# Kernel optimization log

Measured on AMD Instinct MI355X. Metric: run time of the kernel, lower is better.

## Reference

```python
import jax, jax.numpy as jnp
import numpy as np

N = 10000
E = 320000
NFEAT = 512
NHID = 256
NCLASS = 64
N_LAYERS = 8
ALPHA = 0.1
THETA = 0.5
BN_EPS = 1e-5


def setup_inputs() -> dict:
    key = jax.random.key(0)
    k = jax.random.split(key, 6)
    return {
        "x": jax.random.normal(k[0], (N, NFEAT), jnp.float32),
        "edge_index": jax.random.randint(k[1], (2, E), 0, N, dtype=jnp.int32),
        "lin0_w": jax.random.normal(k[2], (NFEAT, NHID), jnp.float32) * float(1.0 / np.sqrt(NFEAT)),
        "lin0_b": jnp.zeros((NHID,), jnp.float32),
        "lin1_w": jax.random.normal(k[3], (NHID, NCLASS), jnp.float32) * float(1.0 / np.sqrt(NHID)),
        "lin1_b": jnp.zeros((NCLASS,), jnp.float32),
        "conv_w": jax.random.normal(k[4], (N_LAYERS, NHID, NHID), jnp.float32) * float(1.0 / np.sqrt(NHID)),
        "bn_gamma": jnp.ones((N_LAYERS, NHID), jnp.float32),
        "bn_beta": jnp.zeros((N_LAYERS, NHID), jnp.float32),
    }


def reference(x, edge_index, lin0_w, lin0_b, lin1_w, lin1_b, conv_w, bn_gamma, bn_beta):
    # gcn_norm with self-loops: D^{-1/2} (A + I) D^{-1/2}
    loops = jnp.arange(N, dtype=edge_index.dtype)
    row = jnp.concatenate([edge_index[0], loops])
    col = jnp.concatenate([edge_index[1], loops])
    deg = jax.ops.segment_sum(jnp.ones_like(row, dtype=x.dtype), col, num_segments=N)
    dinv = jnp.where(deg > 0, jax.lax.rsqrt(jnp.maximum(deg, 1e-12)), 0.0)
    ew = dinv[row] * dinv[col]  # [E+N] edge weights

    def spmm(h):
        # adj_t built with (row=col, col=row): out[col[e]] += w[e] * h[row[e]]
        return jax.ops.segment_sum(ew[:, None] * h[row], col, num_segments=N)

    h = jax.nn.relu(x @ lin0_w + lin0_b)  # [N, NHID]
    x0 = h

    layer_idx = jnp.arange(1, N_LAYERS + 1, dtype=x.dtype)
    betas = jnp.log(THETA / layer_idx + 1.0)  # GCN2Conv beta per layer

    def step(h, layer):
        Wl, g, b, beta = layer
        p = spmm(h)
        p = (1.0 - ALPHA) * p + ALPHA * x0  # initial residual blend
        out = (1.0 - beta) * p + beta * (p @ Wl)  # identity mapping
        mu = out.mean(axis=0)
        var = out.var(axis=0)
        out = (out - mu) * jax.lax.rsqrt(var + BN_EPS) * g + b
        return jax.nn.relu(out), None

    h, _ = jax.lax.scan(step, h, (conv_w, bn_gamma, bn_beta, betas))
    return h @ lin1_w + lin1_b  # [N, NCLASS]
```

## Files before the change

kernel.cpp:

```cpp
#include <hip/hip_runtime.h>
#include <hip/hip_fp16.h>
#include <math.h>

#define N_NODES 10000
#define N_EDGES 320000
#define NFEAT 512
#define NHID 256
#define NCLASS 64
#define N_LAYERS 8
#define BN_EPS 1e-5f

typedef unsigned short u16;
typedef __attribute__((ext_vector_type(8))) short short8v;
typedef __attribute__((ext_vector_type(4))) float f32x4;

__device__ __forceinline__ u16 bf_hi_bits(float f) {
    unsigned u = __float_as_uint(f);
    unsigned r = (u + 0x7fffu + ((u >> 16) & 1u)) >> 16;
    return (u16)r;
}
__device__ __forceinline__ float bf_to_f(u16 h) {
    return __uint_as_float(((unsigned)h) << 16);
}
__device__ __forceinline__ float4 loadh4(const __half* p) {
    float2 raw = *(const float2*)p;
    __half2 h0 = *reinterpret_cast<const __half2*>(&raw.x);
    __half2 h1 = *reinterpret_cast<const __half2*>(&raw.y);
    float2 f0 = __half22float2(h0);
    float2 f1 = __half22float2(h1);
    return make_float4(f0.x, f0.y, f1.x, f1.y);
}
__device__ __forceinline__ void storeh4(__half* p, float4 v) {
    __half2 h0 = __float22half2_rn(make_float2(v.x, v.y));
    __half2 h1 = __float22half2_rn(make_float2(v.z, v.w));
    float2 raw;
    raw.x = *reinterpret_cast<float*>(&h0);
    raw.y = *reinterpret_cast<float*>(&h1);
    *(float2*)p = raw;
}

__global__ void init_kernel(int* __restrict__ deg, int* __restrict__ cursor,
                            float* __restrict__ stats) {
    int i = blockIdx.x * 256 + threadIdx.x;
    if (i < N_NODES) { deg[i] = 1; cursor[i] = 0; }
    if (i < N_LAYERS * 2 * NHID) stats[i] = 0.f;
}

__global__ void deg_count(const int* __restrict__ col, int* __restrict__ deg) {
    int e = blockIdx.x * 256 + threadIdx.x;
    if (e < N_EDGES) atomicAdd(&deg[col[e]], 1);
}

__global__ void dinv_kernel(const int* __restrict__ deg, float* __restrict__ dinv) {
    int i = blockIdx.x * 256 + threadIdx.x;
    if (i < N_NODES) dinv[i] = rsqrtf((float)deg[i]);
}

__global__ void scan_kernel(const int* __restrict__ deg, int* __restrict__ offs) {
    __shared__ int sm[256];
    __shared__ int carry_s;
    int tid = threadIdx.x;
    if (tid == 0) carry_s = 0;
    __syncthreads();
    for (int base = 0; base < N_NODES; base += 256) {
        int i = base + tid;
        int cnt = (i < N_NODES) ? (deg[i] - 1) : 0;
        sm[tid] = cnt;
        __syncthreads();
        #pragma unroll
        for (int off = 1; off < 256; off <<= 1) {
            int v = (tid >= off) ? sm[tid - off] : 0;
            __syncthreads();
            sm[tid] += v;
            __syncthreads();
        }
        int excl = sm[tid] - cnt;
        int carry = carry_s;
        if (i < N_NODES) offs[i] = carry + excl;
        int total = sm[255];
        __syncthreads();
        if (tid == 0) carry_s = carry + total;
        __syncthreads();
    }
    if (tid == 0) offs[N_NODES] = carry_s;
}

__global__ void scatter_kernel(const int* __restrict__ row, const int* __restrict__ col,
                               const float* __restrict__ dinv, const int* __restrict__ offs,
                               int* __restrict__ cursor, int2* __restrict__ csr) {
    int e = blockIdx.x * 256 + threadIdx.x;
    if (e >= N_EDGES) return;
    int c = col[e], r = row[e];
    int pos = offs[c] + atomicAdd(&cursor[c], 1);
    float w = dinv[r] * dinv[c];
    csr[pos] = make_int2(r, __float_as_int(w));
}

__global__ void convert_x(const float4* __restrict__ x4, ushort4* __restrict__ xh,
                          ushort4* __restrict__ xl) {
    int i = blockIdx.x * 256 + threadIdx.x;
    if (i >= N_NODES * NFEAT / 4) return;
    float4 v = x4[i];
    ushort4 h, l;
    h.x = bf_hi_bits(v.x); l.x = bf_hi_bits(v.x - bf_to_f(h.x));
    h.y = bf_hi_bits(v.y); l.y = bf_hi_bits(v.y - bf_to_f(h.y));
    h.z = bf_hi_bits(v.z); l.z = bf_hi_bits(v.z - bf_to_f(h.z));
    h.w = bf_hi_bits(v.w); l.w = bf_hi_bits(v.w - bf_to_f(h.w));
    xh[i] = h; xl[i] = l;
}

__global__ void convert_w(const float* __restrict__ cw, u16* __restrict__ wh, u16* __restrict__ wl,
                          const float* __restrict__ l0w, u16* __restrict__ w0h, u16* __restrict__ w0l) {
    int i = blockIdx.x * 256 + threadIdx.x;
    if (i < N_LAYERS * NHID * NHID) {
        int l = i >> 16, rem = i & 65535, n = rem & 255;
        float f = cw[i];
        u16 h = bf_hi_bits(f); u16 lo = bf_hi_bits(f - bf_to_f(h));
        int o = (l << 16) | (n << 8) | (rem >> 8);
        wh[o] = h; wl[o] = lo;
    } else {
        int j = i - N_LAYERS * NHID * NHID;
        if (j < NFEAT * NHID) {
            int k = j >> 8, n = j & 255;
            float f = l0w[j];
            u16 h = bf_hi_bits(f); u16 lo = bf_hi_bits(f - bf_to_f(h));
            int o = n * NFEAT + k;
            w0h[o] = h; w0l[o] = lo;
        }
    }
}

__global__ __launch_bounds__(256)
void spmm_blend(const __half* __restrict__ hb, const __half* __restrict__ x0b,
                const int* __restrict__ offs, const int2* __restrict__ csr,
                const float* __restrict__ dinv,
                ushort4* __restrict__ ph, ushort4* __restrict__ pl) {
    int wid = threadIdx.x >> 6;
    int lane = threadIdx.x & 63;
    int v = blockIdx.x * 4 + wid;
    if (v >= N_NODES) return;
    int f0 = lane * 4;
    size_t base = (size_t)v * NHID + f0;
    float dv = dinv[v];
    float sw = dv * dv;
    float4 a0 = loadh4(hb + base);
    a0.x *= sw; a0.y *= sw; a0.z *= sw; a0.w *= sw;
    float4 a1 = make_float4(0.f, 0.f, 0.f, 0.f);
    int beg = offs[v], end = offs[v + 1];
    int e = beg;
    for (; e + 1 < end; e += 2) {
        int2 s0 = csr[e];
        int2 s1 = csr[e + 1];
        float w0 = __int_as_float(s0.y);
        float w1 = __int_as_float(s1.y);
        float4 h0 = loadh4(hb + (size_t)s0.x * NHID + f0);
        float4 h1 = loadh4(hb + (size_t)s1.x * NHID + f0);
        a0.x = fmaf(w0, h0.x, a0.x); a1.x = fmaf(w1, h1.x, a1.x);
        a0.y = fmaf(w0, h0.y, a0.y); a1.y = fmaf(w1, h1.y, a1.y);
        a0.z = fmaf(w0, h0.z, a0.z); a1.z = fmaf(w1, h1.z, a1.z);
        a0.w = fmaf(w0, h0.w, a0.w); a1.w = fmaf(w1, h1.w, a1.w);
    }
    if (e < end) {
        int2 s0 = csr[e];
        float w0 = __int_as_float(s0.y);
        float4 h0 = loadh4(hb + (size_t)s0.x * NHID + f0);
        a0.x = fmaf(w0, h0.x, a0.x);
        a0.y = fmaf(w0, h0.y, a0.y);
        a0.z = fmaf(w0, h0.z, a0.z);
        a0.w = fmaf(w0, h0.w, a0.w);
    }
    float4 xv = loadh4(x0b + base);
    float4 r;
    r.x = 0.9f * (a0.x + a1.x) + 0.1f * xv.x;
    r.y = 0.9f * (a0.y + a1.y) + 0.1f * xv.y;
    r.z = 0.9f * (a0.z + a1.z) + 0.1f * xv.z;
    r.w = 0.9f * (a0.w + a1.w) + 0.1f * xv.w;
    ushort4 hh, ll;
    hh.x = bf_hi_bits(r.x); ll.x = bf_hi_bits(r.x - bf_to_f(hh.x));
    hh.y = bf_hi_bits(r.y); ll.y = bf_hi_bits(r.y - bf_to_f(hh.y));
    hh.z = bf_hi_bits(r.z); ll.z = bf_hi_bits(r.z - bf_to_f(hh.z));
    hh.w = bf_hi_bits(r.w); ll.w = bf_hi_bits(r.w - bf_to_f(hh.w));
    ph[(size_t)v * 64 + lane] = hh;
    pl[(size_t)v * 64 + lane] = ll;
}

template<int MODE>
__global__ __launch_bounds__(256)
void gemm_mfma(const u16* __restrict__ Ah, const u16* __restrict__ Al,
               const u16* __restrict__ BTh, const u16* __restrict__ BTl,
               const float* __restrict__ bias, __half* __restrict__ C,
               float* __restrict__ stats, int M, int K,
               float alpha, float rcoef) {
    __shared__ u16 As_h[64][40], As_l[64][40];
    __shared__ u16 Bs_h[128][40], Bs_l[128][40];
    int tid = threadIdx.x;
    int lane = tid & 63, wid = tid >> 6;
    int wr = wid >> 1, wc = wid & 1;
    int brow = blockIdx.x * 64;
    int bcol = blockIdx.y * 128;

    f32x4 acc[2][4];
    #pragma unroll
    for (int i = 0; i < 2; ++i)
        #pragma unroll
        for (int j = 0; j < 4; ++j) { acc[i][j].x = 0.f; acc[i][j].y = 0.f; acc[i][j].z = 0.f; acc[i][j].w = 0.f; }

    int am = tid >> 2, akc = (tid & 3) * 8;
    int bn = tid >> 1, bkc = (tid & 1) * 16;
    bool aval = (brow + am) < M;
    size_t arow_off = (size_t)(brow + am) * K + akc;
    size_t brow_off = (size_t)(bcol + bn) * K + bkc;
    int rlo = lane & 15, kg = (lane >> 4) * 8;

    for (int k0 = 0; k0 < K; k0 += 32) {
        uint4 z4 = make_uint4(0, 0, 0, 0);
        uint4 a_h = aval ? *(const uint4*)(Ah + arow_off + k0) : z4;
        uint4 a_l = aval ? *(const uint4*)(Al + arow_off + k0) : z4;
        uint4 b_h0 = *(const uint4*)(BTh + brow_off + k0);
        uint4 b_h1 = *(const uint4*)(BTh + brow_off + k0 + 8);
        uint4 b_l0 = *(const uint4*)(BTl + brow_off + k0);
        uint4 b_l1 = *(const uint4*)(BTl + brow_off + k0 + 8);
        __syncthreads();
        *(uint4*)&As_h[am][akc] = a_h;
        *(uint4*)&As_l[am][akc] = a_l;
        *(uint4*)&Bs_h[bn][bkc] = b_h0;
        *(uint4*)&Bs_h[bn][bkc + 8] = b_h1;
        *(uint4*)&Bs_l[bn][bkc] = b_l0;
        *(uint4*)&Bs_l[bn][bkc + 8] = b_l1;
        __syncthreads();

        short8v afh[2], afl[2], bfh[4], bfl[4];
        #pragma unroll
        for (int mf = 0; mf < 2; ++mf) {
            afh[mf] = *(const short8v*)&As_h[wr * 32 + mf * 16 + rlo][kg];
            afl[mf] = *(const short8v*)&As_l[wr * 32 + mf * 16 + rlo][kg];
        }
        #pragma unroll
        for (int nf = 0; nf < 4; ++nf) {
            bfh[nf] = *(const short8v*)&Bs_h[wc * 64 + nf * 16 + rlo][kg];
            bfl[nf] = *(const short8v*)&Bs_l[wc * 64 + nf * 16 + rlo][kg];
        }
        #pragma unroll
        for (int mf = 0; mf < 2; ++mf)
            #pragma unroll
            for (int nf = 0; nf < 4; ++nf) {
                acc[mf][nf] = __builtin_amdgcn_mfma_f32_16x16x32_bf16(afl[mf], bfh[nf], acc[mf][nf], 0, 0, 0);
                acc[mf][nf] = __builtin_amdgcn_mfma_f32_16x16x32_bf16(afh[mf], bfl[nf], acc[mf][nf], 0, 0, 0);
                acc[mf][nf] = __builtin_amdgcn_mfma_f32_16x16x32_bf16(afh[mf], bfh[nf], acc[mf][nf], 0, 0, 0);
            }
    }

    int r0 = brow + wr * 32 + (lane >> 4) * 4;
    #pragma unroll
    for (int nf = 0; nf < 4; ++nf) {
        int c = bcol + wc * 64 + nf * 16 + rlo;
        float s = 0.f, s2 = 0.f;
        float bv = (MODE == 0) ? bias[c] : 0.f;
        #pragma unroll
        for (int mf = 0; mf < 2; ++mf) {
            #pragma unroll
            for (int reg = 0; reg < 4; ++reg) {
                int rr = r0 + mf * 16 + reg;
                if (rr < M) {
                    float o;
                    if (MODE == 0) {
                        o = fmaxf(acc[mf][nf][reg] + bv, 0.f);
                    } else {
                        size_t pi = (size_t)rr * K + c;
                        float p = bf_to_f(Ah[pi]) + bf_to_f(Al[pi]);
                        o = alpha * acc[mf][nf][reg] + rcoef * p;
                        s += o; s2 = fmaf(o, o, s2);
                    }
                    C[(size_t)rr * NHID + c] = __float2half(o);
                }
            }
        }
        if (MODE == 1) {
            s  += __shfl_xor(s, 16);  s  += __shfl_xor(s, 32);
            s2 += __shfl_xor(s2, 16); s2 += __shfl_xor(s2, 32);
            if (lane < 16) {
                atomicAdd(&stats[c], s);
                atomicAdd(&stats[NHID + c], s2);
            }
        }
    }
}

__global__ __launch_bounds__(256)
void gemm_lin1(const __half* __restrict__ A, const float* __restrict__ B,
               const float* __restrict__ bias, float* __restrict__ C,
               int M, int Nc, int K) {
    __shared__ float As[16][68];
    __shared__ float Bs[16][68];
    int tid = threadIdx.x;
    int tc = tid & 15, tr = tid >> 4;
    int brow = blockIdx.x * 64, bcol = blockIdx.y * 64;
    float acc[4][4] = {};
    int arow = tid >> 2;
    int ak = (tid & 3) * 4;
    int bkrow = tid >> 4;
    int bcol4 = (tid & 15) * 4;

    for (int k0 = 0; k0 < K; k0 += 16) {
        int gr = brow + arow;
        float4 av = (gr < M) ? loadh4(A + (size_t)gr * K + k0 + ak)
                             : make_float4(0.f, 0.f, 0.f, 0.f);
        As[ak + 0][arow] = av.x;
        As[ak + 1][arow] = av.y;
        As[ak + 2][arow] = av.z;
        As[ak + 3][arow] = av.w;
        float4 bv = *(const float4*)&B[(size_t)(k0 + bkrow) * Nc + bcol + bcol4];
        *(float4*)&Bs[bkrow][bcol4] = bv;
        __syncthreads();
        #pragma unroll
        for (int kk = 0; kk < 16; ++kk) {
            float4 a = *(const float4*)&As[kk][tr * 4];
            float4 b = *(const float4*)&Bs[kk][tc * 4];
            acc[0][0] = fmaf(a.x, b.x, acc[0][0]);
            acc[0][1] = fmaf(a.x, b.y, acc[0][1]);
            acc[0][2] = fmaf(a.x, b.z, acc[0][2]);
            acc[0][3] = fmaf(a.x, b.w, acc[0][3]);
            acc[1][0] = fmaf(a.y, b.x, acc[1][0]);
            acc[1][1] = fmaf(a.y, b.y, acc[1][1]);
            acc[1][2] = fmaf(a.y, b.z, acc[1][2]);
            acc[1][3] = fmaf(a.y, b.w, acc[1][3]);
            acc[2][0] = fmaf(a.z, b.x, acc[2][0]);
            acc[2][1] = fmaf(a.z, b.y, acc[2][1]);
            acc[2][2] = fmaf(a.z, b.z, acc[2][2]);
            acc[2][3] = fmaf(a.z, b.w, acc[2][3]);
            acc[3][0] = fmaf(a.w, b.x, acc[3][0]);
            acc[3][1] = fmaf(a.w, b.y, acc[3][1]);
            acc[3][2] = fmaf(a.w, b.z, acc[3][2]);
            acc[3][3] = fmaf(a.w, b.w, acc[3][3]);
        }
        __syncthreads();
    }

    int r0 = brow + tr * 4, c0 = bcol + tc * 4;
    float4 b4 = *(const float4*)&bias[c0];
    #pragma unroll
    for (int i = 0; i < 4; ++i) {
        int r = r0 + i;
        if (r >= M) continue;
        float4 o;
        o.x = acc[i][0] + b4.x;
        o.y = acc[i][1] + b4.y;
        o.z = acc[i][2] + b4.z;
        o.w = acc[i][3] + b4.w;
        *(float4*)&C[(size_t)r * Nc + c0] = o;
    }
}

__global__ void bn_final(const float* __restrict__ stats, const float* __restrict__ g,
                         const float* __restrict__ b, float* __restrict__ AB) {
    int f = threadIdx.x;
    float mu = stats[f] * (1.f / N_NODES);
    float var = stats[NHID + f] * (1.f / N_NODES) - mu * mu;
    float rs = rsqrtf(var + BN_EPS);
    float a = g[f] * rs;
    AB[f] = a;
    AB[NHID + f] = b[f] - mu * a;
}

__global__ __launch_bounds__(256)
void bn_apply(const __half* __restrict__ outh, const float* __restrict__ AB,
              __half* __restrict__ hb) {
    int i = blockIdx.x * 256 + threadIdx.x;
    if (i >= N_NODES * 64) return;
    int f4 = (i & 63) * 4;
    float4 v = loadh4(outh + (size_t)i * 4);
    float4 r;
    r.x = fmaxf(fmaf(v.x, AB[f4 + 0], AB[NHID + f4 + 0]), 0.f);
    r.y = fmaxf(fmaf(v.y, AB[f4 + 1], AB[NHID + f4 + 1]), 0.f);
    r.z = fmaxf(fmaf(v.z, AB[f4 + 2], AB[NHID + f4 + 2]), 0.f);
    r.w = fmaxf(fmaf(v.w, AB[f4 + 3], AB[NHID + f4 + 3]), 0.f);
    storeh4(hb + (size_t)i * 4, r);
}

static inline size_t align_up(size_t x, size_t a) { return (x + a - 1) & ~(a - 1); }

extern "C" void kernel_launch(void* const* d_in, const int* in_sizes, int n_in,
                              void* d_out, int out_size, void* d_ws, size_t ws_size,
                              hipStream_t stream) {
    const float* x       = (const float*)d_in[0];
    const int*   ei      = (const int*)d_in[1];
    const float* lin0_w  = (const float*)d_in[2];
    const float* lin0_b  = (const float*)d_in[3];
    const float* lin1_w  = (const float*)d_in[4];
    const float* lin1_b  = (const float*)d_in[5];
    const float* conv_w  = (const float*)d_in[6];
    const float* bn_g    = (const float*)d_in[7];
    const float* bn_b    = (const float*)d_in[8];
    const int* rowp = ei;
    const int* colp = ei + N_EDGES;
    float* outp = (float*)d_out;

    char* ws = (char*)d_ws;
    size_t off = 0;
    auto alloc = [&](size_t bytes) { size_t o = off; off = align_up(off + bytes, 256); return ws + o; };
    int*    deg    = (int*)alloc(N_NODES * 4);
    int*    cursor = (int*)alloc(N_NODES * 4);
    int*    offs   = (int*)alloc((N_NODES + 1) * 4);
    float*  dinv   = (float*)alloc(N_NODES * 4);
    int2*   csr    = (int2*)alloc((size_t)N_EDGES * 8);
    __half* x0     = (__half*)alloc((size_t)N_NODES * NHID * 2);
    __half* hbuf   = (__half*)alloc((size_t)N_NODES * NHID * 2);
    __half* outb   = (__half*)alloc((size_t)N_NODES * NHID * 2);
    float*  stats  = (float*)alloc(N_LAYERS * 2 * NHID * 4);
    float*  AB     = (float*)alloc(2 * NHID * 4);
    u16*    xh     = (u16*)alloc((size_t)N_NODES * NFEAT * 2);
    u16*    xl     = (u16*)alloc((size_t)N_NODES * NFEAT * 2);
    u16*    wh     = (u16*)alloc((size_t)N_LAYERS * NHID * NHID * 2);
    u16*    wl     = (u16*)alloc((size_t)N_LAYERS * NHID * NHID * 2);
    u16*    w0h    = (u16*)alloc((size_t)NFEAT * NHID * 2);
    u16*    w0l    = (u16*)alloc((size_t)NFEAT * NHID * 2);
    (void)ws_size; (void)n_in; (void)in_sizes; (void)out_size;

    init_kernel<<<40, 256, 0, stream>>>(deg, cursor, stats);
    deg_count<<<(N_EDGES + 255) / 256, 256, 0, stream>>>(colp, deg);
    dinv_kernel<<<(N_NODES + 255) / 256, 256, 0, stream>>>(deg, dinv);
    scan_kernel<<<1, 256, 0, stream>>>(deg, offs);
    scatter_kernel<<<(N_EDGES + 255) / 256, 256, 0, stream>>>(rowp, colp, dinv, offs, cursor, csr);

    convert_w<<<(N_LAYERS * NHID * NHID + NFEAT * NHID + 255) / 256, 256, 0, stream>>>(
        conv_w, wh, wl, lin0_w, w0h, w0l);
    convert_x<<<(N_NODES * NFEAT / 4 + 255) / 256, 256, 0, stream>>>(
        (const float4*)x, (ushort4*)xh, (ushort4*)xl);

    gemm_mfma<0><<<dim3(157, 2), 256, 0, stream>>>(
        xh, xl, w0h, w0l, lin0_b, x0, nullptr, N_NODES, NFEAT, 1.f, 0.f);

    u16* ph = xh;
    u16* pl = xl;

    const __half* h_in = x0;
    for (int l = 0; l < N_LAYERS; ++l) {
        float beta = logf(0.5f / (float)(l + 1) + 1.0f);
        spmm_blend<<<2500, 256, 0, stream>>>(
            h_in, x0, offs, csr, dinv, (ushort4*)ph, (ushort4*)pl);
        gemm_mfma<1><<<dim3(157, 2), 256, 0, stream>>>(
            ph, pl, wh + (size_t)l * NHID * NHID, wl + (size_t)l * NHID * NHID,
            nullptr, outb, stats + l * 2 * NHID, N_NODES, NHID, beta, 1.f - beta);
        bn_final<<<1, 256, 0, stream>>>(stats + l * 2 * NHID, bn_g + l * NHID, bn_b + l * NHID, AB);
        bn_apply<<<2500, 256, 0, stream>>>(outb, AB, hbuf);
        h_in = hbuf;
    }

    gemm_lin1<<<dim3(157, 1), 256, 0, stream>>>(
        hbuf, lin1_w, lin1_b, outp, N_NODES, NCLASS, NHID);
}
```

Baseline: 729.6 us.

## Fuse BatchNorm finalize and apply into SpMM gather and final linear

Removes the per-layer bn_final and bn_apply kernels. The BN affine transform and ReLU are now applied on the fly to gathered neighbor rows inside the SpMM, and to the A operand in the final lin1 GEMM. This saves a full read/write pass over the hidden activations and two launches per layer, but redoes the BN math per gathered edge (about 32 neighbors per node on average). The single-block degree scan is also rewritten to a chunked per-thread scan with a single block-level pass.

```diff
diff --git a/kernel.cpp b/kernel.cpp
--- a/kernel.cpp
+++ b/kernel.cpp
@@ -30,14 +30,6 @@
     float2 f1 = __half22float2(h1);
     return make_float4(f0.x, f0.y, f1.x, f1.y);
 }
-__device__ __forceinline__ void storeh4(__half* p, float4 v) {
-    __half2 h0 = __float22half2_rn(make_float2(v.x, v.y));
-    __half2 h1 = __float22half2_rn(make_float2(v.z, v.w));
-    float2 raw;
-    raw.x = *reinterpret_cast<float*>(&h0);
-    raw.y = *reinterpret_cast<float*>(&h1);
-    *(float2*)p = raw;
-}
 
 __global__ void init_kernel(int* __restrict__ deg, int* __restrict__ cursor,
                             float* __restrict__ stats) {
@@ -56,33 +48,36 @@
     if (i < N_NODES) dinv[i] = rsqrtf((float)deg[i]);
 }
 
+#define SCAN_CHUNK 40
 __global__ void scan_kernel(const int* __restrict__ deg, int* __restrict__ offs) {
-    __shared__ int sm[256];
-    __shared__ int carry_s;
+    __shared__ int tsum[256];
     int tid = threadIdx.x;
-    if (tid == 0) carry_s = 0;
+    int base = tid * SCAN_CHUNK;
+    int local[SCAN_CHUNK];
+    int s = 0;
+    #pragma unroll
+    for (int j = 0; j < SCAN_CHUNK; ++j) {
+        int i = base + j;
+        int v = (i < N_NODES) ? (deg[i] - 1) : 0;
+        local[j] = s;
+        s += v;
+    }
+    tsum[tid] = s;
     __syncthreads();
-    for (int base = 0; base < N_NODES; base += 256) {
-        int i = base + tid;
-        int cnt = (i < N_NODES) ? (deg[i] - 1) : 0;
-        sm[tid] = cnt;
-        __syncthreads();
-        #pragma unroll
-        for (int off = 1; off < 256; off <<= 1) {
-            int v = (tid >= off) ? sm[tid - off] : 0;
-            __syncthreads();
-            sm[tid] += v;
-            __syncthreads();
-        }
-        int excl = sm[tid] - cnt;
-        int carry = carry_s;
-        if (i < N_NODES) offs[i] = carry + excl;
-        int total = sm[255];
-        __syncthreads();
-        if (tid == 0) carry_s = carry + total;
-        __syncthreads();
-    }
-    if (tid == 0) offs[N_NODES] = carry_s;
+    #pragma unroll
+    for (int off = 1; off < 256; off <<= 1) {
+        int v = (tid >= off) ? tsum[tid - off] : 0;
+        __syncthreads();
+        tsum[tid] += v;
+        __syncthreads();
+    }
+    int carry = (tid > 0) ? tsum[tid - 1] : 0;
+    #pragma unroll
+    for (int j = 0; j < SCAN_CHUNK; ++j) {
+        int i = base + j;
+        if (i < N_NODES) offs[i] = carry + local[j];
+    }
+    if (tid == 255) offs[N_NODES] = tsum[255];
 }
 
 __global__ void scatter_kernel(const int* __restrict__ row, const int* __restrict__ col,
@@ -130,20 +125,56 @@
     }
 }
 
+template<int BN>
 __global__ __launch_bounds__(256)
-void spmm_blend(const __half* __restrict__ hb, const __half* __restrict__ x0b,
+void spmm_blend(const __half* __restrict__ src, const __half* __restrict__ x0b,
                 const int* __restrict__ offs, const int2* __restrict__ csr,
                 const float* __restrict__ dinv,
+                const float* __restrict__ stats, const float* __restrict__ g,
+                const float* __restrict__ b,
                 ushort4* __restrict__ ph, ushort4* __restrict__ pl) {
     int wid = threadIdx.x >> 6;
     int lane = threadIdx.x & 63;
     int v = blockIdx.x * 4 + wid;
     if (v >= N_NODES) return;
     int f0 = lane * 4;
+
+    float4 A4 = make_float4(1.f, 1.f, 1.f, 1.f);
+    float4 B4 = make_float4(0.f, 0.f, 0.f, 0.f);
+    if (BN) {
+        float4 sv = *(const float4*)&stats[f0];
+        float4 qv = *(const float4*)&stats[NHID + f0];
+        float4 gv = *(const float4*)&g[f0];
+        float4 bv = *(const float4*)&b[f0];
+        const float inv = 1.f / N_NODES;
+        float mu, var, rs;
+        mu = sv.x * inv; var = qv.x * inv - mu * mu; rs = rsqrtf(var + BN_EPS);
+        A4.x = gv.x * rs; B4.x = bv.x - mu * A4.x;
+        mu = sv.y * inv; var = qv.y * inv - mu * mu; rs = rsqrtf(var + BN_EPS);
+        A4.y = gv.y * rs; B4.y = bv.y - mu * A4.y;
+        mu = sv.z * inv; var = qv.z * inv - mu * mu; rs = rsqrtf(var + BN_EPS);
+        A4.z = gv.z * rs; B4.z = bv.z - mu * A4.z;
+        mu = sv.w * inv; var = qv.w * inv - mu * mu; rs = rsqrtf(var + BN_EPS);
+        A4.w = gv.w * rs; B4.w = bv.w - mu * A4.w;
+    }
+    auto tf = [&](float4 r) {
+        float4 o;
+        if (BN) {
+            o.x = fmaxf(fmaf(r.x, A4.x, B4.x), 0.f);
+            o.y = fmaxf(fmaf(r.y, A4.y, B4.y), 0.f);
+            o.z = fmaxf(fmaf(r.z, A4.z, B4.z), 0.f);
+            o.w = fmaxf(fmaf(r.w, A4.w, B4.w), 0.f);
+        } else {
+            o.x = fmaxf(r.x, 0.f); o.y = fmaxf(r.y, 0.f);
+            o.z = fmaxf(r.z, 0.f); o.w = fmaxf(r.w, 0.f);
+        }
+        return o;
+    };
+
     size_t base = (size_t)v * NHID + f0;
     float dv = dinv[v];
     float sw = dv * dv;
-    float4 a0 = loadh4(hb + base);
+    float4 a0 = tf(loadh4(src + base));
     a0.x *= sw; a0.y *= sw; a0.z *= sw; a0.w *= sw;
     float4 a1 = make_float4(0.f, 0.f, 0.f, 0.f);
     int beg = offs[v], end = offs[v + 1];
@@ -153,8 +184,8 @@
         int2 s1 = csr[e + 1];
         float w0 = __int_as_float(s0.y);
         float w1 = __int_as_float(s1.y);
-        float4 h0 = loadh4(hb + (size_t)s0.x * NHID + f0);
-        float4 h1 = loadh4(hb + (size_t)s1.x * NHID + f0);
+        float4 h0 = tf(loadh4(src + (size_t)s0.x * NHID + f0));
+        float4 h1 = tf(loadh4(src + (size_t)s1.x * NHID + f0));
         a0.x = fmaf(w0, h0.x, a0.x); a1.x = fmaf(w1, h1.x, a1.x);
         a0.y = fmaf(w0, h0.y, a0.y); a1.y = fmaf(w1, h1.y, a1.y);
         a0.z = fmaf(w0, h0.z, a0.z); a1.z = fmaf(w1, h1.z, a1.z);
@@ -163,7 +194,7 @@
     if (e < end) {
         int2 s0 = csr[e];
         float w0 = __int_as_float(s0.y);
-        float4 h0 = loadh4(hb + (size_t)s0.x * NHID + f0);
+        float4 h0 = tf(loadh4(src + (size_t)s0.x * NHID + f0));
         a0.x = fmaf(w0, h0.x, a0.x);
         a0.y = fmaf(w0, h0.y, a0.y);
         a0.z = fmaf(w0, h0.z, a0.z);
@@ -289,10 +320,22 @@
 __global__ __launch_bounds__(256)
 void gemm_lin1(const __half* __restrict__ A, const float* __restrict__ B,
                const float* __restrict__ bias, float* __restrict__ C,
+               const float* __restrict__ stats, const float* __restrict__ g,
+               const float* __restrict__ b,
                int M, int Nc, int K) {
     __shared__ float As[16][68];
     __shared__ float Bs[16][68];
+    __shared__ float ABs[2][NHID];
     int tid = threadIdx.x;
+    {
+        float mu = stats[tid] * (1.f / N_NODES);
+        float var = stats[NHID + tid] * (1.f / N_NODES) - mu * mu;
+        float rs = rsqrtf(var + BN_EPS);
+        float a = g[tid] * rs;
+        ABs[0][tid] = a;
+        ABs[1][tid] = b[tid] - mu * a;
+    }
+    __syncthreads();
     int tc = tid & 15, tr = tid >> 4;
     int brow = blockIdx.x * 64, bcol = blockIdx.y * 64;
     float acc[4][4] = {};
@@ -305,6 +348,10 @@
         int gr = brow + arow;
         float4 av = (gr < M) ? loadh4(A + (size_t)gr * K + k0 + ak)
                              : make_float4(0.f, 0.f, 0.f, 0.f);
+        av.x = fmaxf(fmaf(av.x, ABs[0][k0 + ak + 0], ABs[1][k0 + ak + 0]), 0.f);
+        av.y = fmaxf(fmaf(av.y, ABs[0][k0 + ak + 1], ABs[1][k0 + ak + 1]), 0.f);
+        av.z = fmaxf(fmaf(av.z, ABs[0][k0 + ak + 2], ABs[1][k0 + ak + 2]), 0.f);
+        av.w = fmaxf(fmaf(av.w, ABs[0][k0 + ak + 3], ABs[1][k0 + ak + 3]), 0.f);
         As[ak + 0][arow] = av.x;
         As[ak + 1][arow] = av.y;
         As[ak + 2][arow] = av.z;
@@ -315,23 +362,23 @@
         #pragma unroll
         for (int kk = 0; kk < 16; ++kk) {
             float4 a = *(const float4*)&As[kk][tr * 4];
-            float4 b = *(const float4*)&Bs[kk][tc * 4];
-            acc[0][0] = fmaf(a.x, b.x, acc[0][0]);
-            acc[0][1] = fmaf(a.x, b.y, acc[0][1]);
-            acc[0][2] = fmaf(a.x, b.z, acc[0][2]);
-            acc[0][3] = fmaf(a.x, b.w, acc[0][3]);
-            acc[1][0] = fmaf(a.y, b.x, acc[1][0]);
-            acc[1][1] = fmaf(a.y, b.y, acc[1][1]);
-            acc[1][2] = fmaf(a.y, b.z, acc[1][2]);
-            acc[1][3] = fmaf(a.y, b.w, acc[1][3]);
-            acc[2][0] = fmaf(a.z, b.x, acc[2][0]);
-            acc[2][1] = fmaf(a.z, b.y, acc[2][1]);
-            acc[2][2] = fmaf(a.z, b.z, acc[2][2]);
-            acc[2][3] = fmaf(a.z, b.w, acc[2][3]);
-            acc[3][0] = fmaf(a.w, b.x, acc[3][0]);
-            acc[3][1] = fmaf(a.w, b.y, acc[3][1]);
-            acc[3][2] = fmaf(a.w, b.z, acc[3][2]);
-            acc[3][3] = fmaf(a.w, b.w, acc[3][3]);
+            float4 b2 = *(const float4*)&Bs[kk][tc * 4];
+            acc[0][0] = fmaf(a.x, b2.x, acc[0][0]);
+            acc[0][1] = fmaf(a.x, b2.y, acc[0][1]);
+            acc[0][2] = fmaf(a.x, b2.z, acc[0][2]);
+            acc[0][3] = fmaf(a.x, b2.w, acc[0][3]);
+            acc[1][0] = fmaf(a.y, b2.x, acc[1][0]);
+            acc[1][1] = fmaf(a.y, b2.y, acc[1][1]);
+            acc[1][2] = fmaf(a.y, b2.z, acc[1][2]);
+            acc[1][3] = fmaf(a.y, b2.w, acc[1][3]);
+            acc[2][0] = fmaf(a.z, b2.x, acc[2][0]);
+            acc[2][1] = fmaf(a.z, b2.y, acc[2][1]);
+            acc[2][2] = fmaf(a.z, b2.z, acc[2][2]);
+            acc[2][3] = fmaf(a.z, b2.w, acc[2][3]);
+            acc[3][0] = fmaf(a.w, b2.x, acc[3][0]);
+            acc[3][1] = fmaf(a.w, b2.y, acc[3][1]);
+            acc[3][2] = fmaf(a.w, b2.z, acc[3][2]);
+            acc[3][3] = fmaf(a.w, b2.w, acc[3][3]);
         }
         __syncthreads();
     }
@@ -349,32 +396,6 @@
         o.w = acc[i][3] + b4.w;
         *(float4*)&C[(size_t)r * Nc + c0] = o;
     }
-}
-
-__global__ void bn_final(const float* __restrict__ stats, const float* __restrict__ g,
-                         const float* __restrict__ b, float* __restrict__ AB) {
-    int f = threadIdx.x;
-    float mu = stats[f] * (1.f / N_NODES);
-    float var = stats[NHID + f] * (1.f / N_NODES) - mu * mu;
-    float rs = rsqrtf(var + BN_EPS);
-    float a = g[f] * rs;
-    AB[f] = a;
-    AB[NHID + f] = b[f] - mu * a;
-}
-
-__global__ __launch_bounds__(256)
-void bn_apply(const __half* __restrict__ outh, const float* __restrict__ AB,
-              __half* __restrict__ hb) {
-    int i = blockIdx.x * 256 + threadIdx.x;
-    if (i >= N_NODES * 64) return;
-    int f4 = (i & 63) * 4;
-    float4 v = loadh4(outh + (size_t)i * 4);
-    float4 r;
-    r.x = fmaxf(fmaf(v.x, AB[f4 + 0], AB[NHID + f4 + 0]), 0.f);
-    r.y = fmaxf(fmaf(v.y, AB[f4 + 1], AB[NHID + f4 + 1]), 0.f);
-    r.z = fmaxf(fmaf(v.z, AB[f4 + 2], AB[NHID + f4 + 2]), 0.f);
-    r.w = fmaxf(fmaf(v.w, AB[f4 + 3], AB[NHID + f4 + 3]), 0.f);
-    storeh4(hb + (size_t)i * 4, r);
 }
 
 static inline size_t align_up(size_t x, size_t a) { return (x + a - 1) & ~(a - 1); }
@@ -404,10 +425,8 @@
     float*  dinv   = (float*)alloc(N_NODES * 4);
     int2*   csr    = (int2*)alloc((size_t)N_EDGES * 8);
     __half* x0     = (__half*)alloc((size_t)N_NODES * NHID * 2);
-    __half* hbuf   = (__half*)alloc((size_t)N_NODES * NHID * 2);
     __half* outb   = (__half*)alloc((size_t)N_NODES * NHID * 2);
     float*  stats  = (float*)alloc(N_LAYERS * 2 * NHID * 4);
-    float*  AB     = (float*)alloc(2 * NHID * 4);
     u16*    xh     = (u16*)alloc((size_t)N_NODES * NFEAT * 2);
     u16*    xl     = (u16*)alloc((size_t)N_NODES * NFEAT * 2);
     u16*    wh     = (u16*)alloc((size_t)N_LAYERS * NHID * NHID * 2);
@@ -433,19 +452,25 @@
     u16* ph = xh;
     u16* pl = xl;
 
-    const __half* h_in = x0;
     for (int l = 0; l < N_LAYERS; ++l) {
         float beta = logf(0.5f / (float)(l + 1) + 1.0f);
-        spmm_blend<<<2500, 256, 0, stream>>>(
-            h_in, x0, offs, csr, dinv, (ushort4*)ph, (ushort4*)pl);
+        if (l == 0) {
+            spmm_blend<0><<<2500, 256, 0, stream>>>(
+                x0, x0, offs, csr, dinv, nullptr, nullptr, nullptr,
+                (ushort4*)ph, (ushort4*)pl);
+        } else {
+            spmm_blend<1><<<2500, 256, 0, stream>>>(
+                outb, x0, offs, csr, dinv,
+                stats + (l - 1) * 2 * NHID, bn_g + (l - 1) * NHID, bn_b + (l - 1) * NHID,
+                (ushort4*)ph, (ushort4*)pl);
+        }
         gemm_mfma<1><<<dim3(157, 2), 256, 0, stream>>>(
             ph, pl, wh + (size_t)l * NHID * NHID, wl + (size_t)l * NHID * NHID,
             nullptr, outb, stats + l * 2 * NHID, N_NODES, NHID, beta, 1.f - beta);
-        bn_final<<<1, 256, 0, stream>>>(stats + l * 2 * NHID, bn_g + l * NHID, bn_b + l * NHID, AB);
-        bn_apply<<<2500, 256, 0, stream>>>(outb, AB, hbuf);
-        h_in = hbuf;
     }
 
     gemm_lin1<<<dim3(157, 1), 256, 0, stream>>>(
-        hbuf, lin1_w, lin1_b, outp, N_NODES, NCLASS, NHID);
-}
+        outb, lin1_w, lin1_b, outp,
+        stats + 7 * 2 * NHID, bn_g + 7 * NHID, bn_b + 7 * NHID,
+        N_NODES, NCLASS, NHID);
+}
```

Measured after the change: 654.9 us. 10.2% less time.
